# Kernel tuning notes

Hardware: AMD Instinct MI355X
Metric: run time of the kernel (lower is better)

## Reference

```python
import jax, jax.numpy as jnp
import numpy as np

N_NODES = 20000
LN_EPS = 1e-5


def setup_inputs() -> dict:
    key = jax.random.key(0)
    ks = jax.random.split(key, 8)
    N, E, D_IN, D_H = N_NODES, 320000, 128, 256
    x = jax.random.normal(ks[0], (N, D_IN), dtype=jnp.float32)
    edge_index = jax.random.randint(ks[1], (2, E), 0, N, dtype=jnp.int64)
    edge_weight = jax.random.uniform(ks[2], (E,), dtype=jnp.float32)
    # Glorot-ish scaled weights
    W1 = jax.random.normal(ks[3], (D_IN, D_H), dtype=jnp.float32) / np.sqrt(D_IN)
    W2 = jax.random.normal(ks[4], (D_H, D_H), dtype=jnp.float32) / np.sqrt(D_H)
    Wres = jax.random.normal(ks[5], (D_IN, D_H), dtype=jnp.float32) / np.sqrt(D_IN)
    return {
        "x": x, "edge_index": edge_index, "edge_weight": edge_weight,
        "W1": W1, "b1": jnp.zeros((D_H,), jnp.float32),
        "W2": W2, "b2": jnp.zeros((D_H,), jnp.float32),
        "Wres": Wres, "bres": jnp.zeros((D_H,), jnp.float32),
        "gamma1": jnp.ones((D_H,), jnp.float32), "beta1": jnp.zeros((D_H,), jnp.float32),
        "gamma2": jnp.ones((D_H,), jnp.float32), "beta2": jnp.zeros((D_H,), jnp.float32),
    }


def _gcn_conv(x, W, b, src, dst, w, n):
    # PyG GCNConv: linear transform, then sym-normalized scatter-add aggregation
    h = x @ W  # [N, D_H]
    deg = jax.ops.segment_sum(w, dst, num_segments=n)  # in-degree incl. self loops
    dinv = jnp.where(deg > 0, jax.lax.rsqrt(deg), 0.0)
    norm = dinv[src] * w * dinv[dst]  # [E+N]
    out = jax.ops.segment_sum(norm[:, None] * h[src], dst, num_segments=n)
    return out + b


def _layer_norm(x, gamma, beta):
    mu = jnp.mean(x, axis=-1, keepdims=True)
    var = jnp.mean(jnp.square(x - mu), axis=-1, keepdims=True)
    return (x - mu) * jax.lax.rsqrt(var + LN_EPS) * gamma + beta


def reference(x, edge_index, edge_weight, W1, b1, W2, b2, Wres, bres,
              gamma1, beta1, gamma2, beta2):
    n = x.shape[0]
    loop = jnp.arange(n, dtype=edge_index.dtype)
    # add self loops with weight 1 (add_self_loops=True)
    src = jnp.concatenate([edge_index[0], loop])
    dst = jnp.concatenate([edge_index[1], loop])
    w = jnp.concatenate([edge_weight, jnp.ones((n,), edge_weight.dtype)])

    # hop 0: conv -> relu (dropout p=0, eval) -> residual proj -> LayerNorm
    delta = jax.nn.relu(_gcn_conv(x, W1, b1, src, dst, w, n))
    h = _layer_norm(x @ Wres + bres + delta, gamma1, beta1)

    # hop 1 (last): conv -> residual -> LayerNorm (no relu)
    delta = _gcn_conv(h, W2, b2, src, dst, w, n)
    h = _layer_norm(h + delta, gamma2, beta2)
    return h
```

## Files before the change

### kernel.cpp

```cpp
#include <hip/hip_runtime.h>
#include <stdint.h>


constexpr int DIN = 128;
constexpr int DH  = 256;
#define LN_EPS 1e-5f

typedef __attribute__((ext_vector_type(8))) short bf16x8;
typedef __attribute__((ext_vector_type(4))) short bf16x4;
typedef __attribute__((ext_vector_type(4))) float f32x4;

__device__ __forceinline__ short f2bf(float f) {
  union { float f; unsigned u; } v; v.f = f;
  unsigned r = v.u + 0x7fffu + ((v.u >> 16) & 1u);
  return (short)(r >> 16);
}
__device__ __forceinline__ float bf2f(short b) {
  union { unsigned u; float f; } v; v.u = ((unsigned)(unsigned short)b) << 16;
  return v.f;
}


__global__ void k_init(float* deg, int* flag, int n) {
  int i = blockIdx.x * blockDim.x + threadIdx.x;
  if (i < n) deg[i] = 1.0f;
  if (i == 0) *flag = 1;
}

__global__ void k_detect(const unsigned* ei, int nsample, int* flag) {
  int i = blockIdx.x * blockDim.x + threadIdx.x;
  if (i < nsample && ei[2 * i + 1] != 0u) *flag = 0;
}

__device__ __forceinline__ int eidx(const void* ei, long long e, int m64) {
  return m64 ? (int)((const long long*)ei)[e] : ((const int*)ei)[e];
}

__global__ void k_edge_accum(const void* ei, const float* w, float* deg,
                             int* cnt, const int* flag, int E) {
  int e = blockIdx.x * blockDim.x + threadIdx.x;
  if (e >= E) return;
  int m64 = *flag;
  int d = eidx(ei, (long long)E + e, m64);
  atomicAdd(&deg[d], w[e]);
  atomicAdd(&cnt[d], 1);
}

__global__ void k_dinv(float* deg, int n) {
  int i = blockIdx.x * blockDim.x + threadIdx.x;
  if (i < n) deg[i] = rsqrtf(deg[i]);
}

__global__ void k_scan(const int* cnt, int* rowptr, int n) {
  __shared__ int buf[1024];
  __shared__ int carry_s;
  int tid = threadIdx.x;
  if (tid == 0) { carry_s = 0; rowptr[0] = 0; }
  __syncthreads();
  int nchunk = (n + 1023) / 1024;
  for (int c = 0; c < nchunk; ++c) {
    int i = c * 1024 + tid;
    int v = (i < n) ? cnt[i] : 0;
    buf[tid] = v;
    __syncthreads();
    for (int off = 1; off < 1024; off <<= 1) {
      int t = (tid >= off) ? buf[tid - off] : 0;
      __syncthreads();
      buf[tid] += t;
      __syncthreads();
    }
    int total = buf[1023];
    int inc = buf[tid] + carry_s;
    if (i < n) rowptr[i + 1] = inc;
    __syncthreads();
    if (tid == 0) carry_s += total;
    __syncthreads();
  }
}

__global__ void k_cursor(const int* rowptr, int* cursor, int n) {
  int i = blockIdx.x * blockDim.x + threadIdx.x;
  if (i < n) cursor[i] = rowptr[i];
}

__global__ void k_fill(const void* ei, const float* w, const float* dinv,
                       int* cursor, int* srcs, float* norms, const int* flag,
                       int E) {
  int e = blockIdx.x * blockDim.x + threadIdx.x;
  if (e >= E) return;
  int m64 = *flag;
  int s = eidx(ei, e, m64);
  int d = eidx(ei, (long long)E + e, m64);
  int p = atomicAdd(&cursor[d], 1);
  srcs[p] = s;
  norms[p] = dinv[s] * w[e] * dinv[d];
}

__global__ void k_cvt(const float* in, short* out, int n) {
  int i = blockIdx.x * blockDim.x + threadIdx.x;
  if (i < n) out[i] = f2bf(in[i]);
}

__global__ void k_transpose_cvt(const float* W, short* Wt, int K) {
  int idx = blockIdx.x * blockDim.x + threadIdx.x;
  if (idx < K * DH) {
    int k = idx / DH, n = idx % DH;
    Wt[n * K + k] = f2bf(W[idx]);
  }
}


template <int K, bool BF16OUT, bool BIAS>
__global__ __launch_bounds__(256) void k_gemm(const short* __restrict__ A,
                                              const short* __restrict__ Bt,
                                              const float* __restrict__ bias,
                                              short* __restrict__ outb,
                                              float* __restrict__ outf, int M) {
  int tid = threadIdx.x;
  int wave = tid >> 6, lane = tid & 63;
  int lr = lane & 15, lg = lane >> 4;
  int bm = blockIdx.x * 64 + (wave >> 1) * 32;
  int bn = blockIdx.y * 64 + (wave & 1) * 32;

  int r0 = min(bm + lr, M - 1);
  int r1 = min(bm + 16 + lr, M - 1);
  const short* a0p = A + (long long)r0 * K + lg * 8;
  const short* a1p = A + (long long)r1 * K + lg * 8;
  const short* b0p = Bt + (long long)(bn + lr) * K + lg * 8;
  const short* b1p = Bt + (long long)(bn + 16 + lr) * K + lg * 8;

  f32x4 acc[2][2] = {};
#pragma unroll
  for (int ks = 0; ks < K / 32; ++ks) {
    bf16x8 a0 = *(const bf16x8*)(a0p + ks * 32);
    bf16x8 a1 = *(const bf16x8*)(a1p + ks * 32);
    bf16x8 b0 = *(const bf16x8*)(b0p + ks * 32);
    bf16x8 b1 = *(const bf16x8*)(b1p + ks * 32);
    acc[0][0] = __builtin_amdgcn_mfma_f32_16x16x32_bf16(a0, b0, acc[0][0], 0, 0, 0);
    acc[0][1] = __builtin_amdgcn_mfma_f32_16x16x32_bf16(a0, b1, acc[0][1], 0, 0, 0);
    acc[1][0] = __builtin_amdgcn_mfma_f32_16x16x32_bf16(a1, b0, acc[1][0], 0, 0, 0);
    acc[1][1] = __builtin_amdgcn_mfma_f32_16x16x32_bf16(a1, b1, acc[1][1], 0, 0, 0);
  }

#pragma unroll
  for (int mi = 0; mi < 2; ++mi)
#pragma unroll
    for (int ni = 0; ni < 2; ++ni)
#pragma unroll
      for (int j = 0; j < 4; ++j) {
        int row = bm + mi * 16 + lg * 4 + j;
        int col = bn + ni * 16 + lr;
        if (row < M) {
          float v = acc[mi][ni][j];
          if (BIAS) v += bias[col];
          if (BF16OUT) outb[(long long)row * DH + col] = f2bf(v);
          else         outf[(long long)row * DH + col] = v;
        }
      }
}


template <bool RELU>
__global__ __launch_bounds__(64) void k_agg_ln(
    const short* __restrict__ H, const float* __restrict__ resid,
    const float* __restrict__ bias, const float* __restrict__ gamma,
    const float* __restrict__ beta, const int* __restrict__ rowptr,
    const int* __restrict__ srcs, const float* __restrict__ norms,
    const float* __restrict__ dinv, float* __restrict__ out_f,
    short* __restrict__ out_bf, int n) {
  int i = blockIdx.x;
  int lane = threadIdx.x;
  int d = lane * 4;

  float di = dinv[i];
  float acc0, acc1, acc2, acc3;
  {
    bf16x4 hv = *(const bf16x4*)(H + (long long)i * DH + d);
    float sw = di * di;
    acc0 = sw * bf2f(hv[0]); acc1 = sw * bf2f(hv[1]);
    acc2 = sw * bf2f(hv[2]); acc3 = sw * bf2f(hv[3]);
  }
  int e = rowptr[i], end = rowptr[i + 1];
  for (; e < end; ++e) {
    int s = srcs[e];
    float nm = norms[e];
    bf16x4 v = *(const bf16x4*)(H + (long long)s * DH + d);
    acc0 += nm * bf2f(v[0]); acc1 += nm * bf2f(v[1]);
    acc2 += nm * bf2f(v[2]); acc3 += nm * bf2f(v[3]);
  }

  f32x4 rv = *(const f32x4*)(resid + (long long)i * DH + d);
  f32x4 bv = *(const f32x4*)(bias + d);
  float t0 = acc0 + bv[0], t1 = acc1 + bv[1], t2 = acc2 + bv[2], t3 = acc3 + bv[3];
  if (RELU) {
    t0 = fmaxf(t0, 0.f); t1 = fmaxf(t1, 0.f);
    t2 = fmaxf(t2, 0.f); t3 = fmaxf(t3, 0.f);
  }
  t0 += rv[0]; t1 += rv[1]; t2 += rv[2]; t3 += rv[3];

  float s1 = t0 + t1 + t2 + t3;
  float s2 = t0 * t0 + t1 * t1 + t2 * t2 + t3 * t3;
  for (int m = 1; m < 64; m <<= 1) {
    s1 += __shfl_xor(s1, m, 64);
    s2 += __shfl_xor(s2, m, 64);
  }
  float mu = s1 * (1.f / 256.f);
  float var = s2 * (1.f / 256.f) - mu * mu;
  float rs = rsqrtf(var + LN_EPS);

  f32x4 gv = *(const f32x4*)(gamma + d);
  f32x4 be = *(const f32x4*)(beta + d);
  f32x4 y;
  y[0] = (t0 - mu) * rs * gv[0] + be[0];
  y[1] = (t1 - mu) * rs * gv[1] + be[1];
  y[2] = (t2 - mu) * rs * gv[2] + be[2];
  y[3] = (t3 - mu) * rs * gv[3] + be[3];
  *(f32x4*)(out_f + (long long)i * DH + d) = y;
  if (out_bf) {
    bf16x4 ob;
    ob[0] = f2bf(y[0]); ob[1] = f2bf(y[1]);
    ob[2] = f2bf(y[2]); ob[3] = f2bf(y[3]);
    *(bf16x4*)(out_bf + (long long)i * DH + d) = ob;
  }
}


extern "C" void kernel_launch(void* const* d_in, const int* in_sizes, int n_in,
                              void* d_out, int out_size, void* d_ws,
                              size_t ws_size, hipStream_t stream) {
  const float* x    = (const float*)d_in[0];
  const void*  ei   = d_in[1];
  const float* ew   = (const float*)d_in[2];
  const float* W1   = (const float*)d_in[3];
  const float* b1   = (const float*)d_in[4];
  const float* W2   = (const float*)d_in[5];
  const float* b2   = (const float*)d_in[6];
  const float* Wres = (const float*)d_in[7];
  const float* bres = (const float*)d_in[8];
  const float* g1   = (const float*)d_in[9];
  const float* be1  = (const float*)d_in[10];
  const float* g2   = (const float*)d_in[11];
  const float* be2  = (const float*)d_in[12];

  const int N = in_sizes[0] / DIN;
  const int E = in_sizes[2];

  char* ws = (char*)d_ws;
  auto alloc = [&](size_t bytes) -> char* {
    char* p = ws;
    ws += (bytes + 255) & ~(size_t)255;
    return p;
  };
  short* xb     = (short*)alloc((size_t)N * DIN * 2);
  short* W1t    = (short*)alloc((size_t)DIN * DH * 2);
  short* Wrt    = (short*)alloc((size_t)DIN * DH * 2);
  short* W2t    = (short*)alloc((size_t)DH * DH * 2);
  short* Hb     = (short*)alloc((size_t)N * DH * 2);
  float* RES    = (float*)alloc((size_t)N * DH * 4);
  float* h1f    = (float*)alloc((size_t)N * DH * 4);
  short* h1b    = (short*)alloc((size_t)N * DH * 2);
  float* deg    = (float*)alloc((size_t)N * 4);
  int*   cnt    = (int*)alloc((size_t)N * 4);
  int*   rowptr = (int*)alloc((size_t)(N + 1) * 4);
  int*   cursor = (int*)alloc((size_t)N * 4);
  int*   srcs   = (int*)alloc((size_t)E * 4);
  float* norms  = (float*)alloc((size_t)E * 4);
  int*   flag   = (int*)alloc(256);

  const int nb = (N + 255) / 256;
  const int eb = (E + 255) / 256;

  hipMemsetAsync(cnt, 0, (size_t)N * 4, stream);
  k_init<<<nb, 256, 0, stream>>>(deg, flag, N);
  k_detect<<<16, 256, 0, stream>>>((const unsigned*)ei, 4096, flag);
  k_edge_accum<<<eb, 256, 0, stream>>>(ei, ew, deg, cnt, flag, E);
  k_dinv<<<nb, 256, 0, stream>>>(deg, N);
  k_scan<<<1, 1024, 0, stream>>>(cnt, rowptr, N);
  k_cursor<<<nb, 256, 0, stream>>>(rowptr, cursor, N);
  k_fill<<<eb, 256, 0, stream>>>(ei, ew, deg, cursor, srcs, norms, flag, E);

  k_cvt<<<(N * DIN + 255) / 256, 256, 0, stream>>>(x, xb, N * DIN);
  k_transpose_cvt<<<(DIN * DH + 255) / 256, 256, 0, stream>>>(W1, W1t, DIN);
  k_transpose_cvt<<<(DIN * DH + 255) / 256, 256, 0, stream>>>(Wres, Wrt, DIN);
  k_transpose_cvt<<<(DH * DH + 255) / 256, 256, 0, stream>>>(W2, W2t, DH);

  dim3 gg((N + 63) / 64, DH / 64);
  k_gemm<DIN, true, false><<<gg, 256, 0, stream>>>(xb, W1t, nullptr, Hb, nullptr, N);
  k_gemm<DIN, false, true><<<gg, 256, 0, stream>>>(xb, Wrt, bres, nullptr, RES, N);
  k_agg_ln<true><<<N, 64, 0, stream>>>(Hb, RES, b1, g1, be1, rowptr, srcs,
                                       norms, deg, h1f, h1b, N);
  k_gemm<DH, true, false><<<gg, 256, 0, stream>>>(h1b, W2t, nullptr, Hb, nullptr, N);
  k_agg_ln<false><<<N, 64, 0, stream>>>(Hb, h1f, b2, g2, be2, rowptr, srcs,
                                        norms, deg, (float*)d_out, nullptr, N);
}
```

Before: 302.5 us.

## Fuse prep kernels, merge layer-1 GEMMs, wave-scan, and pack agg rows per block

Collapses the many small setup kernels (init, detect, cvt, transposes, dinv, cursor) into fewer launches. The index-width check is now done in-kernel with a wave ballot, and the dinv computation plus cursor init are folded into a shuffle-based scan. The two layer-1 GEMMs are merged so x tiles are loaded once. The aggregation kernel now processes four nodes per 256-thread block with a 4-way unrolled edge loop for more memory-level parallelism. This cuts launch overhead and redundant loads but makes each kernel more complex, and the ballot probe reads only a few sampled words of edge_index.

```diff
diff --git a/kernel.cpp b/kernel.cpp
--- a/kernel.cpp
+++ b/kernel.cpp
@@ -20,75 +20,121 @@
   return v.f;
 }
 
-
-__global__ void k_init(float* deg, int* flag, int n) {
-  int i = blockIdx.x * blockDim.x + threadIdx.x;
-  if (i < n) deg[i] = 1.0f;
-  if (i == 0) *flag = 1;
-}
-
-__global__ void k_detect(const unsigned* ei, int nsample, int* flag) {
-  int i = blockIdx.x * blockDim.x + threadIdx.x;
-  if (i < nsample && ei[2 * i + 1] != 0u) *flag = 0;
+__device__ __forceinline__ int probe_m64(const unsigned* ei) {
+  int lane = threadIdx.x & 63;
+  unsigned v = ei[2 * (lane * 32) + 1];
+  return __ballot(v != 0u) == 0ull;
 }
 
 __device__ __forceinline__ int eidx(const void* ei, long long e, int m64) {
   return m64 ? (int)((const long long*)ei)[e] : ((const int*)ei)[e];
 }
 
-__global__ void k_edge_accum(const void* ei, const float* w, float* deg,
-                             int* cnt, const int* flag, int E) {
-  int e = blockIdx.x * blockDim.x + threadIdx.x;
+
+__global__ __launch_bounds__(256) void k_prep(const float* __restrict__ x,
+                                              short* __restrict__ xb,
+                                              const float* __restrict__ W1,
+                                              const float* __restrict__ Wres,
+                                              const float* __restrict__ W2,
+                                              short* __restrict__ W1t,
+                                              short* __restrict__ Wrt,
+                                              short* __restrict__ W2t,
+                                              float* __restrict__ deg,
+                                              int* __restrict__ cnt, int N) {
+  const int NXV = N * DIN / 8;
+  const int NW  = DIN * DH;
+  const int NW2 = DH * DH;
+  int idx = blockIdx.x * 256 + threadIdx.x;
+  if (idx < NXV) {
+    f32x4 a = ((const f32x4*)x)[idx * 2];
+    f32x4 b = ((const f32x4*)x)[idx * 2 + 1];
+    bf16x8 o;
+    o[0] = f2bf(a[0]); o[1] = f2bf(a[1]); o[2] = f2bf(a[2]); o[3] = f2bf(a[3]);
+    o[4] = f2bf(b[0]); o[5] = f2bf(b[1]); o[6] = f2bf(b[2]); o[7] = f2bf(b[3]);
+    ((bf16x8*)xb)[idx] = o;
+    return;
+  }
+  idx -= NXV;
+  if (idx < N) { deg[idx] = 1.0f; cnt[idx] = 0; return; }
+  idx -= N;
+  if (idx < NW) {
+    int n = idx / DIN, k = idx % DIN;
+    W1t[idx] = f2bf(W1[k * DH + n]);
+    return;
+  }
+  idx -= NW;
+  if (idx < NW) {
+    int n = idx / DIN, k = idx % DIN;
+    Wrt[idx] = f2bf(Wres[k * DH + n]);
+    return;
+  }
+  idx -= NW;
+  if (idx < NW2) {
+    int n = idx / DH, k = idx % DH;
+    W2t[idx] = f2bf(W2[k * DH + n]);
+  }
+}
+
+
+__global__ __launch_bounds__(256) void k_edge_accum(const void* ei,
+                                                    const float* __restrict__ w,
+                                                    float* deg, int* cnt, int E) {
+  int m64 = probe_m64((const unsigned*)ei);
+  int e = blockIdx.x * 256 + threadIdx.x;
   if (e >= E) return;
-  int m64 = *flag;
   int d = eidx(ei, (long long)E + e, m64);
   atomicAdd(&deg[d], w[e]);
   atomicAdd(&cnt[d], 1);
 }
 
-__global__ void k_dinv(float* deg, int n) {
-  int i = blockIdx.x * blockDim.x + threadIdx.x;
-  if (i < n) deg[i] = rsqrtf(deg[i]);
-}
-
-__global__ void k_scan(const int* cnt, int* rowptr, int n) {
-  __shared__ int buf[1024];
+
+__global__ __launch_bounds__(1024) void k_scan(const int* __restrict__ cnt,
+                                               float* deg, int* rowptr,
+                                               int* cursor, int n) {
+  for (int i = threadIdx.x; i < n; i += 1024) deg[i] = rsqrtf(deg[i]);
+
+  __shared__ int wsum[16];
   __shared__ int carry_s;
-  int tid = threadIdx.x;
-  if (tid == 0) { carry_s = 0; rowptr[0] = 0; }
+  int tid = threadIdx.x, lane = tid & 63, wv = tid >> 6;
+  if (tid == 0) { carry_s = 0; rowptr[0] = 0; cursor[0] = 0; }
   __syncthreads();
-  int nchunk = (n + 1023) / 1024;
-  for (int c = 0; c < nchunk; ++c) {
-    int i = c * 1024 + tid;
-    int v = (i < n) ? cnt[i] : 0;
-    buf[tid] = v;
+  for (int c0 = 0; c0 < n; c0 += 1024) {
+    int i = c0 + tid;
+    int sc = (i < n) ? cnt[i] : 0;
+#pragma unroll
+    for (int off = 1; off < 64; off <<= 1) {
+      int t = __shfl_up(sc, off, 64);
+      if (lane >= off) sc += t;
+    }
+    if (lane == 63) wsum[wv] = sc;
     __syncthreads();
-    for (int off = 1; off < 1024; off <<= 1) {
-      int t = (tid >= off) ? buf[tid - off] : 0;
-      __syncthreads();
-      buf[tid] += t;
-      __syncthreads();
+    if (wv == 0) {
+      int s = (lane < 16) ? wsum[lane] : 0;
+#pragma unroll
+      for (int off = 1; off < 16; off <<= 1) {
+        int t = __shfl_up(s, off, 64);
+        if (lane >= off) s += t;
+      }
+      if (lane < 16) wsum[lane] = s;
     }
-    int total = buf[1023];
-    int inc = buf[tid] + carry_s;
-    if (i < n) rowptr[i + 1] = inc;
     __syncthreads();
-    if (tid == 0) carry_s += total;
+    int inc = sc + ((wv > 0) ? wsum[wv - 1] : 0) + carry_s;
+    if (i < n) { rowptr[i + 1] = inc; cursor[i + 1] = inc; }
     __syncthreads();
-  }
-}
-
-__global__ void k_cursor(const int* rowptr, int* cursor, int n) {
-  int i = blockIdx.x * blockDim.x + threadIdx.x;
-  if (i < n) cursor[i] = rowptr[i];
-}
-
-__global__ void k_fill(const void* ei, const float* w, const float* dinv,
-                       int* cursor, int* srcs, float* norms, const int* flag,
-                       int E) {
-  int e = blockIdx.x * blockDim.x + threadIdx.x;
+    if (tid == 0) carry_s += wsum[15];
+    __syncthreads();
+  }
+}
+
+
+__global__ __launch_bounds__(256) void k_fill(const void* ei,
+                                              const float* __restrict__ w,
+                                              const float* __restrict__ dinv,
+                                              int* cursor, int* srcs,
+                                              float* norms, int E) {
+  int m64 = probe_m64((const unsigned*)ei);
+  int e = blockIdx.x * 256 + threadIdx.x;
   if (e >= E) return;
-  int m64 = *flag;
   int s = eidx(ei, e, m64);
   int d = eidx(ei, (long long)E + e, m64);
   int p = atomicAdd(&cursor[d], 1);
@@ -96,26 +142,68 @@
   norms[p] = dinv[s] * w[e] * dinv[d];
 }
 
-__global__ void k_cvt(const float* in, short* out, int n) {
-  int i = blockIdx.x * blockDim.x + threadIdx.x;
-  if (i < n) out[i] = f2bf(in[i]);
-}
-
-__global__ void k_transpose_cvt(const float* W, short* Wt, int K) {
-  int idx = blockIdx.x * blockDim.x + threadIdx.x;
-  if (idx < K * DH) {
-    int k = idx / DH, n = idx % DH;
-    Wt[n * K + k] = f2bf(W[idx]);
-  }
-}
-
-
-template <int K, bool BF16OUT, bool BIAS>
-__global__ __launch_bounds__(256) void k_gemm(const short* __restrict__ A,
-                                              const short* __restrict__ Bt,
-                                              const float* __restrict__ bias,
-                                              short* __restrict__ outb,
-                                              float* __restrict__ outf, int M) {
+
+__global__ __launch_bounds__(256) void k_gemm_l1(const short* __restrict__ A,
+                                                 const short* __restrict__ B1,
+                                                 const short* __restrict__ Br,
+                                                 const float* __restrict__ bres,
+                                                 short* __restrict__ H1,
+                                                 float* __restrict__ RES, int M) {
+  constexpr int K = DIN;
+  int tid = threadIdx.x;
+  int wave = tid >> 6, lane = tid & 63;
+  int lr = lane & 15, lg = lane >> 4;
+  int bm = blockIdx.x * 64 + (wave >> 1) * 32;
+  int bn = blockIdx.y * 64 + (wave & 1) * 32;
+
+  int r0 = min(bm + lr, M - 1);
+  int r1 = min(bm + 16 + lr, M - 1);
+  const short* a0p = A + (long long)r0 * K + lg * 8;
+  const short* a1p = A + (long long)r1 * K + lg * 8;
+  const short* b10p = B1 + (long long)(bn + lr) * K + lg * 8;
+  const short* b11p = B1 + (long long)(bn + 16 + lr) * K + lg * 8;
+  const short* br0p = Br + (long long)(bn + lr) * K + lg * 8;
+  const short* br1p = Br + (long long)(bn + 16 + lr) * K + lg * 8;
+
+  f32x4 a1c[2][2] = {}, arc[2][2] = {};
+#pragma unroll
+  for (int ks = 0; ks < K / 32; ++ks) {
+    bf16x8 a0 = *(const bf16x8*)(a0p + ks * 32);
+    bf16x8 a1 = *(const bf16x8*)(a1p + ks * 32);
+    bf16x8 p0 = *(const bf16x8*)(b10p + ks * 32);
+    bf16x8 p1 = *(const bf16x8*)(b11p + ks * 32);
+    bf16x8 q0 = *(const bf16x8*)(br0p + ks * 32);
+    bf16x8 q1 = *(const bf16x8*)(br1p + ks * 32);
+    a1c[0][0] = __builtin_amdgcn_mfma_f32_16x16x32_bf16(a0, p0, a1c[0][0], 0, 0, 0);
+    a1c[0][1] = __builtin_amdgcn_mfma_f32_16x16x32_bf16(a0, p1, a1c[0][1], 0, 0, 0);
+    a1c[1][0] = __builtin_amdgcn_mfma_f32_16x16x32_bf16(a1, p0, a1c[1][0], 0, 0, 0);
+    a1c[1][1] = __builtin_amdgcn_mfma_f32_16x16x32_bf16(a1, p1, a1c[1][1], 0, 0, 0);
+    arc[0][0] = __builtin_amdgcn_mfma_f32_16x16x32_bf16(a0, q0, arc[0][0], 0, 0, 0);
+    arc[0][1] = __builtin_amdgcn_mfma_f32_16x16x32_bf16(a0, q1, arc[0][1], 0, 0, 0);
+    arc[1][0] = __builtin_amdgcn_mfma_f32_16x16x32_bf16(a1, q0, arc[1][0], 0, 0, 0);
+    arc[1][1] = __builtin_amdgcn_mfma_f32_16x16x32_bf16(a1, q1, arc[1][1], 0, 0, 0);
+  }
+
+#pragma unroll
+  for (int mi = 0; mi < 2; ++mi)
+#pragma unroll
+    for (int ni = 0; ni < 2; ++ni)
+#pragma unroll
+      for (int j = 0; j < 4; ++j) {
+        int row = bm + mi * 16 + lg * 4 + j;
+        int col = bn + ni * 16 + lr;
+        if (row < M) {
+          H1[(long long)row * DH + col] = f2bf(a1c[mi][ni][j]);
+          RES[(long long)row * DH + col] = arc[mi][ni][j] + bres[col];
+        }
+      }
+}
+
+
+__global__ __launch_bounds__(256) void k_gemm2(const short* __restrict__ A,
+                                               const short* __restrict__ Bt,
+                                               short* __restrict__ outb, int M) {
+  constexpr int K = DH;
   int tid = threadIdx.x;
   int wave = tid >> 6, lane = tid & 63;
   int lr = lane & 15, lg = lane >> 4;
@@ -150,26 +238,22 @@
       for (int j = 0; j < 4; ++j) {
         int row = bm + mi * 16 + lg * 4 + j;
         int col = bn + ni * 16 + lr;
-        if (row < M) {
-          float v = acc[mi][ni][j];
-          if (BIAS) v += bias[col];
-          if (BF16OUT) outb[(long long)row * DH + col] = f2bf(v);
-          else         outf[(long long)row * DH + col] = v;
-        }
+        if (row < M) outb[(long long)row * DH + col] = f2bf(acc[mi][ni][j]);
       }
 }
 
 
 template <bool RELU>
-__global__ __launch_bounds__(64) void k_agg_ln(
+__global__ __launch_bounds__(256) void k_agg_ln(
     const short* __restrict__ H, const float* __restrict__ resid,
     const float* __restrict__ bias, const float* __restrict__ gamma,
     const float* __restrict__ beta, const int* __restrict__ rowptr,
     const int* __restrict__ srcs, const float* __restrict__ norms,
     const float* __restrict__ dinv, float* __restrict__ out_f,
     short* __restrict__ out_bf, int n) {
-  int i = blockIdx.x;
-  int lane = threadIdx.x;
+  int wv = threadIdx.x >> 6, lane = threadIdx.x & 63;
+  int i = blockIdx.x * 4 + wv;
+  if (i >= n) return;
   int d = lane * 4;
 
   float di = dinv[i];
@@ -181,6 +265,22 @@
     acc2 = sw * bf2f(hv[2]); acc3 = sw * bf2f(hv[3]);
   }
   int e = rowptr[i], end = rowptr[i + 1];
+  for (; e + 4 <= end; e += 4) {
+    int s0 = srcs[e], s1 = srcs[e + 1], s2 = srcs[e + 2], s3 = srcs[e + 3];
+    float n0 = norms[e], n1 = norms[e + 1], n2 = norms[e + 2], n3 = norms[e + 3];
+    bf16x4 v0 = *(const bf16x4*)(H + (long long)s0 * DH + d);
+    bf16x4 v1 = *(const bf16x4*)(H + (long long)s1 * DH + d);
+    bf16x4 v2 = *(const bf16x4*)(H + (long long)s2 * DH + d);
+    bf16x4 v3 = *(const bf16x4*)(H + (long long)s3 * DH + d);
+    acc0 += n0 * bf2f(v0[0]); acc1 += n0 * bf2f(v0[1]);
+    acc2 += n0 * bf2f(v0[2]); acc3 += n0 * bf2f(v0[3]);
+    acc0 += n1 * bf2f(v1[0]); acc1 += n1 * bf2f(v1[1]);
+    acc2 += n1 * bf2f(v1[2]); acc3 += n1 * bf2f(v1[3]);
+    acc0 += n2 * bf2f(v2[0]); acc1 += n2 * bf2f(v2[1]);
+    acc2 += n2 * bf2f(v2[2]); acc3 += n2 * bf2f(v2[3]);
+    acc0 += n3 * bf2f(v3[0]); acc1 += n3 * bf2f(v3[1]);
+    acc2 += n3 * bf2f(v3[2]); acc3 += n3 * bf2f(v3[3]);
+  }
   for (; e < end; ++e) {
     int s = srcs[e];
     float nm = norms[e];
@@ -200,6 +300,7 @@
 
   float s1 = t0 + t1 + t2 + t3;
   float s2 = t0 * t0 + t1 * t1 + t2 * t2 + t3 * t3;
+#pragma unroll
   for (int m = 1; m < 64; m <<= 1) {
     s1 += __shfl_xor(s1, m, 64);
     s2 += __shfl_xor(s2, m, 64);
@@ -262,34 +363,25 @@
   float* deg    = (float*)alloc((size_t)N * 4);
   int*   cnt    = (int*)alloc((size_t)N * 4);
   int*   rowptr = (int*)alloc((size_t)(N + 1) * 4);
-  int*   cursor = (int*)alloc((size_t)N * 4);
+  int*   cursor = (int*)alloc((size_t)(N + 1) * 4);
   int*   srcs   = (int*)alloc((size_t)E * 4);
   float* norms  = (float*)alloc((size_t)E * 4);
-  int*   flag   = (int*)alloc(256);
-
-  const int nb = (N + 255) / 256;
+
   const int eb = (E + 255) / 256;
 
-  hipMemsetAsync(cnt, 0, (size_t)N * 4, stream);
-  k_init<<<nb, 256, 0, stream>>>(deg, flag, N);
-  k_detect<<<16, 256, 0, stream>>>((const unsigned*)ei, 4096, flag);
-  k_edge_accum<<<eb, 256, 0, stream>>>(ei, ew, deg, cnt, flag, E);
-  k_dinv<<<nb, 256, 0, stream>>>(deg, N);
-  k_scan<<<1, 1024, 0, stream>>>(cnt, rowptr, N);
-  k_cursor<<<nb, 256, 0, stream>>>(rowptr, cursor, N);
-  k_fill<<<eb, 256, 0, stream>>>(ei, ew, deg, cursor, srcs, norms, flag, E);
-
-  k_cvt<<<(N * DIN + 255) / 256, 256, 0, stream>>>(x, xb, N * DIN);
-  k_transpose_cvt<<<(DIN * DH + 255) / 256, 256, 0, stream>>>(W1, W1t, DIN);
-  k_transpose_cvt<<<(DIN * DH + 255) / 256, 256, 0, stream>>>(Wres, Wrt, DIN);
-  k_transpose_cvt<<<(DH * DH + 255) / 256, 256, 0, stream>>>(W2, W2t, DH);
+  int prep_items = N * DIN / 8 + N + 2 * DIN * DH + DH * DH;
+  k_prep<<<(prep_items + 255) / 256, 256, 0, stream>>>(
+      x, xb, W1, Wres, W2, W1t, Wrt, W2t, deg, cnt, N);
+  k_edge_accum<<<eb, 256, 0, stream>>>(ei, ew, deg, cnt, E);
+  k_scan<<<1, 1024, 0, stream>>>(cnt, deg, rowptr, cursor, N);
+  k_fill<<<eb, 256, 0, stream>>>(ei, ew, deg, cursor, srcs, norms, E);
 
   dim3 gg((N + 63) / 64, DH / 64);
-  k_gemm<DIN, true, false><<<gg, 256, 0, stream>>>(xb, W1t, nullptr, Hb, nullptr, N);
-  k_gemm<DIN, false, true><<<gg, 256, 0, stream>>>(xb, Wrt, bres, nullptr, RES, N);
-  k_agg_ln<true><<<N, 64, 0, stream>>>(Hb, RES, b1, g1, be1, rowptr, srcs,
-                                       norms, deg, h1f, h1b, N);
-  k_gemm<DH, true, false><<<gg, 256, 0, stream>>>(h1b, W2t, nullptr, Hb, nullptr, N);
-  k_agg_ln<false><<<N, 64, 0, stream>>>(Hb, h1f, b2, g2, be2, rowptr, srcs,
-                                        norms, deg, (float*)d_out, nullptr, N);
-}
+  k_gemm_l1<<<gg, 256, 0, stream>>>(xb, W1t, Wrt, bres, Hb, RES, N);
+  k_agg_ln<true><<<(N + 3) / 4, 256, 0, stream>>>(Hb, RES, b1, g1, be1, rowptr,
+                                                  srcs, norms, deg, h1f, h1b, N);
+  k_gemm2<<<gg, 256, 0, stream>>>(h1b, W2t, Hb, N);
+  k_agg_ln<false><<<(N + 3) / 4, 256, 0, stream>>>(Hb, h1f, b2, g2, be2, rowptr,
+                                                   srcs, norms, deg,
+                                                   (float*)d_out, nullptr, N);
+}
```

Measured after the change: 264.7 us. 12.5% less time.
